# Optimization experiments

Hardware: AMD Instinct MI355X
Metric: run time of the kernel (lower is better)

The kernel has to match this reference:

```python
import jax, jax.numpy as jnp
import numpy as np

N = 1048576          # nodes at current depth (children), divisible by 8
M = N // 8           # non-empty parent nodes (conv outputs)
NNUM_PARENT = 262144 # total parent nodes at depth-1
C_IN = 128
C_OUT = 256


def setup_inputs() -> dict:
    key = jax.random.key(0)
    k1, k2, k3 = jax.random.split(key, 3)
    data = jax.random.normal(k1, (N, C_IN), dtype=jnp.float32)
    weights = jax.random.normal(k2, (8, C_IN, C_OUT), dtype=jnp.float32) * (1.0 / np.sqrt(8 * C_IN))
    # sorted unique positions of non-empty parents within [0, NNUM_PARENT)
    perm = jax.random.permutation(k3, NNUM_PARENT)
    nempty_idx = jnp.sort(perm[:M]).astype(jnp.int32)
    return {"data": data, "weights": weights, "nempty_idx": nempty_idx,
            "nnum_parent": NNUM_PARENT}


def reference(data, weights, nempty_idx, nnum_parent):
    # kernel-2 stride-2 conv: each consecutive group of 8 children -> one parent
    c_in, c_out = weights.shape[1], weights.shape[2]
    out = data.reshape(-1, 8 * c_in) @ weights.reshape(8 * c_in, c_out)  # [M, C_out]
    # octree_pad at depth-1: scatter into all parent nodes, zeros at empty ones
    full = jnp.zeros((nnum_parent, c_out), dtype=out.dtype).at[nempty_idx].set(out)
    return full
```

## Files before the change

### kernel.cpp

```cpp
#include <hip/hip_runtime.h>
#include <hip/hip_bf16.h>

typedef float f32x4 __attribute__((ext_vector_type(4)));
typedef short s16x8 __attribute__((ext_vector_type(8)));

using bf16 = __hip_bfloat16;

namespace {
constexpr int KD = 1024;
constexpr int BM = 128;
constexpr int BK = 32;
constexpr int NT = KD / BK;
constexpr int MBLK = 131072 / BM;
constexpr int ZBLK = 1024;
}

typedef __attribute__((address_space(1))) const void GVoid;
typedef __attribute__((address_space(3))) void LVoid;

__device__ __forceinline__ void gld16(const void* g, void* l) {
  __builtin_amdgcn_global_load_lds((GVoid*)g, (LVoid*)l, 16, 0, 0);
}

__device__ __forceinline__ s16x8 cvt8(f32x4 a, f32x4 b) {
  union { s16x8 v; bf16 h[8]; } u;
#pragma unroll
  for (int j = 0; j < 4; ++j) u.h[j] = __float2bfloat16(a[j]);
#pragma unroll
  for (int j = 0; j < 4; ++j) u.h[j + 4] = __float2bfloat16(b[j]);
  return u.v;
}

__global__ void k_transpose_w(const float* __restrict__ w, bf16* __restrict__ bt) {
  int t = blockIdx.x * 256 + threadIdx.x;
  int n = t & 255;
  int k0 = (t >> 8) << 3;
  union { s16x8 v; bf16 h[8]; } u;
#pragma unroll
  for (int j = 0; j < 8; ++j)
    u.h[j] = __float2bfloat16(w[(size_t)(k0 + j) * 256 + n]);
  *(s16x8*)(bt + (size_t)n * KD + k0) = u.v;
}

__global__ void k_clear_flags(int* __restrict__ flags, int np4) {
  int i = blockIdx.x * 256 + threadIdx.x;
  if (i < np4) ((int4*)flags)[i] = make_int4(0, 0, 0, 0);
}

__global__ void k_set_flags(const int* __restrict__ idx, int* __restrict__ flags, int m) {
  int i = blockIdx.x * 256 + threadIdx.x;
  if (i < m) flags[idx[i]] = 1;
}

__global__ __launch_bounds__(512, 4)
void k_fused(const float* __restrict__ A, const bf16* __restrict__ Bt,
             const int* __restrict__ idx, const int* __restrict__ flags,
             float* __restrict__ out, int NP) {
  __shared__ float As[2][BM * BK];
  __shared__ bf16  Bs[2][256 * BK];

  const int tid = threadIdx.x;
  const int lane = tid & 63;
  const int wave = tid >> 6;

  if (blockIdx.x >= MBLK) {
    const int zb = blockIdx.x - MBLK;
    f32x4 z = {0.f, 0.f, 0.f, 0.f};
    for (int row = zb * 8 + wave; row < NP; row += ZBLK * 8) {
      if (flags[row] == 0)
        *(f32x4*)(out + (size_t)row * 256 + lane * 4) = z;
    }
    return;
  }

  const int m0 = blockIdx.x * BM;
  const int wm = wave >> 2;
  const int wn = wave & 3;

  const int as0 = tid, as1 = 512 + tid;
  const int ar0 = as0 >> 3, ac0 = (as0 & 7) ^ (ar0 & 6);
  const int ar1 = as1 >> 3, ac1 = (as1 & 7) ^ (ar1 & 6);
  const float* aSrc0 = A + (size_t)(m0 + ar0) * KD + ac0 * 4;
  const float* aSrc1 = A + (size_t)(m0 + ar1) * KD + ac1 * 4;
  const int aOff0 = (wave * 64) * 4;
  const int aOff1 = (512 + wave * 64) * 4;

  const int bs0 = tid, bs1 = 512 + tid;
  const int br0 = bs0 >> 2, bc0 = (bs0 & 3) ^ (br0 & 3);
  const int br1 = bs1 >> 2, bc1 = (bs1 & 3) ^ (br1 & 3);
  const bf16* bSrc0 = Bt + (size_t)br0 * KD + bc0 * 8;
  const bf16* bSrc1 = Bt + (size_t)br1 * KD + bc1 * 8;
  const int bOff0 = (wave * 64) * 8;
  const int bOff1 = (512 + wave * 64) * 8;

  const int arow = wm * 64 + (lane & 15);
  const int kc = lane >> 4;
  const int aRd = arow * 32 + (((2 * kc) ^ (arow & 6)) * 4);
  const int brow = wn * 64 + (lane & 15);
  const int bRd = brow * 32 + ((kc ^ (brow & 3)) * 8);

  f32x4 acc[4][4] = {};

  auto stage = [&](int buf, int t) {
    gld16(aSrc0 + t * BK, &As[buf][aOff0]);
    gld16(aSrc1 + t * BK, &As[buf][aOff1]);
    gld16(bSrc0 + t * BK, &Bs[buf][bOff0]);
    gld16(bSrc1 + t * BK, &Bs[buf][bOff1]);
  };

  stage(0, 0);
  __syncthreads();

  int cur = 0;
#pragma unroll 1
  for (int t = 0; t < NT; ++t) {
    if (t + 1 < NT) stage(cur ^ 1, t + 1);

    s16x8 bfr[4];
#pragma unroll
    for (int fn = 0; fn < 4; ++fn)
      bfr[fn] = *(const s16x8*)(&Bs[cur][bRd + fn * 512]);

#pragma unroll
    for (int fm = 0; fm < 4; ++fm) {
      f32x4 lo = *(const f32x4*)(&As[cur][aRd + fm * 512]);
      f32x4 hi = *(const f32x4*)(&As[cur][aRd + fm * 512 + 4]);
      s16x8 af = cvt8(lo, hi);
#pragma unroll
      for (int fn = 0; fn < 4; ++fn)
        acc[fm][fn] = __builtin_amdgcn_mfma_f32_16x16x32_bf16(
            af, bfr[fn], acc[fm][fn], 0, 0, 0);
    }
    __syncthreads();
    cur ^= 1;
  }

  const int col0 = wn * 64 + (lane & 15);
  const int rb = m0 + wm * 64 + ((lane >> 4) << 2);
#pragma unroll
  for (int fm = 0; fm < 4; ++fm) {
#pragma unroll
    for (int j = 0; j < 4; ++j) {
      int orow = idx[rb + fm * 16 + j];
      float* op = out + (size_t)orow * 256 + col0;
#pragma unroll
      for (int fn = 0; fn < 4; ++fn)
        op[fn * 16] = acc[fm][fn][j];
    }
  }
}

extern "C" void kernel_launch(void* const* d_in, const int* in_sizes, int n_in,
                              void* d_out, int out_size, void* d_ws, size_t ws_size,
                              hipStream_t stream) {
  const float* data = (const float*)d_in[0];
  const float* w    = (const float*)d_in[1];
  const int*   idx  = (const int*)d_in[2];
  float* out = (float*)d_out;

  const int M  = in_sizes[2];
  const int NP = out_size / 256;

  int* flags = (int*)d_ws;
  bf16* bt = (bf16*)((char*)d_ws + (size_t)NP * sizeof(int));

  k_transpose_w<<<128, 256, 0, stream>>>(w, bt);
  k_clear_flags<<<(NP / 4 + 255) / 256, 256, 0, stream>>>(flags, NP / 4);
  k_set_flags<<<(M + 255) / 256, 256, 0, stream>>>(idx, flags, M);
  k_fused<<<MBLK + ZBLK, 512, 0, stream>>>(data, bt, idx, flags, out, NP);
}
```

Measured before the change: 253.0 us.

## Drop LDS staging and load GEMM operands directly from global into registers

The fused GEMM kernel stops staging A and B tiles through shared memory with async global-to-LDS loads and double buffering. Each wave now loads its A rows and B columns straight from global memory into registers, and the block tile shrinks to 64 rows with 4 waves of 256 threads. Zero-fill blocks are interleaved with GEMM blocks (every fifth block) instead of being appended at the end, and output row indices are fetched as one int4. This removes LDS traffic and barriers, but all four waves in a block now read the same A rows separately and rely on the cache for reuse, which raises global and L2 load pressure.

```diff
diff --git a/kernel.cpp b/kernel.cpp
--- a/kernel.cpp
+++ b/kernel.cpp
@@ -8,18 +8,8 @@
 
 namespace {
 constexpr int KD = 1024;
-constexpr int BM = 128;
 constexpr int BK = 32;
 constexpr int NT = KD / BK;
-constexpr int MBLK = 131072 / BM;
-constexpr int ZBLK = 1024;
-}
-
-typedef __attribute__((address_space(1))) const void GVoid;
-typedef __attribute__((address_space(3))) void LVoid;
-
-__device__ __forceinline__ void gld16(const void* g, void* l) {
-  __builtin_amdgcn_global_load_lds((GVoid*)g, (LVoid*)l, 16, 0, 0);
 }
 
 __device__ __forceinline__ s16x8 cvt8(f32x4 a, f32x4 b) {
@@ -52,97 +42,65 @@
   if (i < m) flags[idx[i]] = 1;
 }
 
-__global__ __launch_bounds__(512, 4)
+__global__ __launch_bounds__(256, 3)
 void k_fused(const float* __restrict__ A, const bf16* __restrict__ Bt,
              const int* __restrict__ idx, const int* __restrict__ flags,
-             float* __restrict__ out, int NP) {
-  __shared__ float As[2][BM * BK];
-  __shared__ bf16  Bs[2][256 * BK];
+             float* __restrict__ out, int NP, int ZBtot) {
+  const int bid = blockIdx.x;
+  const int lane = threadIdx.x & 63;
+  const int wave = threadIdx.x >> 6;
 
-  const int tid = threadIdx.x;
-  const int lane = tid & 63;
-  const int wave = tid >> 6;
-
-  if (blockIdx.x >= MBLK) {
-    const int zb = blockIdx.x - MBLK;
-    f32x4 z = {0.f, 0.f, 0.f, 0.f};
-    for (int row = zb * 8 + wave; row < NP; row += ZBLK * 8) {
+  if ((bid % 5) == 4) {
+    const int zb = bid / 5;
+    const f32x4 z = {0.f, 0.f, 0.f, 0.f};
+    const int stride = ZBtot * 4;
+    for (int row = zb * 4 + wave; row < NP; row += stride) {
       if (flags[row] == 0)
         *(f32x4*)(out + (size_t)row * 256 + lane * 4) = z;
     }
     return;
   }
 
-  const int m0 = blockIdx.x * BM;
-  const int wm = wave >> 2;
-  const int wn = wave & 3;
+  const int gid = bid - bid / 5;
+  const size_t m0 = (size_t)gid * 64;
+  const int n0 = wave * 64;
 
-  const int as0 = tid, as1 = 512 + tid;
-  const int ar0 = as0 >> 3, ac0 = (as0 & 7) ^ (ar0 & 6);
-  const int ar1 = as1 >> 3, ac1 = (as1 & 7) ^ (ar1 & 6);
-  const float* aSrc0 = A + (size_t)(m0 + ar0) * KD + ac0 * 4;
-  const float* aSrc1 = A + (size_t)(m0 + ar1) * KD + ac1 * 4;
-  const int aOff0 = (wave * 64) * 4;
-  const int aOff1 = (512 + wave * 64) * 4;
+  const int r = lane & 15;
+  const int kc = lane >> 4;
 
-  const int bs0 = tid, bs1 = 512 + tid;
-  const int br0 = bs0 >> 2, bc0 = (bs0 & 3) ^ (br0 & 3);
-  const int br1 = bs1 >> 2, bc1 = (bs1 & 3) ^ (br1 & 3);
-  const bf16* bSrc0 = Bt + (size_t)br0 * KD + bc0 * 8;
-  const bf16* bSrc1 = Bt + (size_t)br1 * KD + bc1 * 8;
-  const int bOff0 = (wave * 64) * 8;
-  const int bOff1 = (512 + wave * 64) * 8;
-
-  const int arow = wm * 64 + (lane & 15);
-  const int kc = lane >> 4;
-  const int aRd = arow * 32 + (((2 * kc) ^ (arow & 6)) * 4);
-  const int brow = wn * 64 + (lane & 15);
-  const int bRd = brow * 32 + ((kc ^ (brow & 3)) * 8);
+  const float* ap = A + (m0 + r) * KD + kc * 8;
+  const bf16*  bp = Bt + (size_t)(n0 + r) * KD + kc * 8;
 
   f32x4 acc[4][4] = {};
 
-  auto stage = [&](int buf, int t) {
-    gld16(aSrc0 + t * BK, &As[buf][aOff0]);
-    gld16(aSrc1 + t * BK, &As[buf][aOff1]);
-    gld16(bSrc0 + t * BK, &Bs[buf][bOff0]);
-    gld16(bSrc1 + t * BK, &Bs[buf][bOff1]);
-  };
-
-  stage(0, 0);
-  __syncthreads();
-
-  int cur = 0;
-#pragma unroll 1
+#pragma unroll 2
   for (int t = 0; t < NT; ++t) {
-    if (t + 1 < NT) stage(cur ^ 1, t + 1);
-
-    s16x8 bfr[4];
+    s16x8 bv[4], av[4];
 #pragma unroll
     for (int fn = 0; fn < 4; ++fn)
-      bfr[fn] = *(const s16x8*)(&Bs[cur][bRd + fn * 512]);
-
+      bv[fn] = *(const s16x8*)(bp + (size_t)fn * 16 * KD + t * BK);
 #pragma unroll
     for (int fm = 0; fm < 4; ++fm) {
-      f32x4 lo = *(const f32x4*)(&As[cur][aRd + fm * 512]);
-      f32x4 hi = *(const f32x4*)(&As[cur][aRd + fm * 512 + 4]);
-      s16x8 af = cvt8(lo, hi);
+      f32x4 lo = *(const f32x4*)(ap + (size_t)fm * 16 * KD + t * BK);
+      f32x4 hi = *(const f32x4*)(ap + (size_t)fm * 16 * KD + t * BK + 4);
+      av[fm] = cvt8(lo, hi);
+    }
+#pragma unroll
+    for (int fm = 0; fm < 4; ++fm)
 #pragma unroll
       for (int fn = 0; fn < 4; ++fn)
         acc[fm][fn] = __builtin_amdgcn_mfma_f32_16x16x32_bf16(
-            af, bfr[fn], acc[fm][fn], 0, 0, 0);
-    }
-    __syncthreads();
-    cur ^= 1;
+            av[fm], bv[fn], acc[fm][fn], 0, 0, 0);
   }
 
-  const int col0 = wn * 64 + (lane & 15);
-  const int rb = m0 + wm * 64 + ((lane >> 4) << 2);
+  const int col0 = n0 + r;
 #pragma unroll
   for (int fm = 0; fm < 4; ++fm) {
+    const int4 rows = *(const int4*)(idx + m0 + fm * 16 + kc * 4);
+    const int rj[4] = {rows.x, rows.y, rows.z, rows.w};
 #pragma unroll
     for (int j = 0; j < 4; ++j) {
-      int orow = idx[rb + fm * 16 + j];
-      float* op = out + (size_t)orow * 256 + col0;
+      float* op = out + (size_t)rj[j] * 256 + col0;
 #pragma unroll
       for (int fn = 0; fn < 4; ++fn)
         op[fn * 16] = acc[fm][fn][j];
@@ -164,8 +122,12 @@
   int* flags = (int*)d_ws;
   bf16* bt = (bf16*)((char*)d_ws + (size_t)NP * sizeof(int));
 
+  const int MT = M / 64;
+  const int ZB = MT / 4;
+  const int TOT = MT + ZB;
+
   k_transpose_w<<<128, 256, 0, stream>>>(w, bt);
   k_clear_flags<<<(NP / 4 + 255) / 256, 256, 0, stream>>>(flags, NP / 4);
   k_set_flags<<<(M + 255) / 256, 256, 0, stream>>>(idx, flags, M);
-  k_fused<<<MBLK + ZBLK, 512, 0, stream>>>(data, bt, idx, flags, out, NP);
+  k_fused<<<TOT, 256, 0, stream>>>(data, bt, idx, flags, out, NP, ZB);
 }
```

After: 501.5 us. 98.2% more time.
